# Optimization experiments

Measured on AMD Instinct MI355X. Metric: run time of the kernel, lower is better.

Reference implementation:

```python
import jax, jax.numpy as jnp
import numpy as np

BS, SEQ_LEN, N_NODES = 16, 12, 512
D, H, L, K = 256, 8, 2, 16
DFF = 4 * D
DH = D // H


def setup_inputs() -> dict:
    key = jax.random.key(0)
    ks = jax.random.split(key, 12)
    p = lambda i, shape: jax.random.normal(ks[i], shape, dtype=jnp.float32) * 0.02
    return dict(
        x_c=jax.random.normal(ks[0], (BS, SEQ_LEN, N_NODES), dtype=jnp.float32),
        A=jax.random.uniform(ks[1], (N_NODES, N_NODES), dtype=jnp.float32),
        W_src_emb=p(2, (SEQ_LEN, D)),
        W_tgt_emb=p(3, (SEQ_LEN, D)),
        enc_attn=p(4, (L, 4, D, D)),
        enc_ffn1=p(5, (L, D, DFF)),
        enc_ffn2=p(6, (L, DFF, D)),
        dec_self=p(7, (L, 4, D, D)),
        dec_cross=p(8, (L, 4, D, D)),
        dec_ffn1=p(9, (L, D, DFF)),
        dec_ffn2=p(10, (L, DFF, D)),
        W_gen=p(11, (D, SEQ_LEN)),
    )


def _ln(x):
    m = jnp.mean(x, axis=-1, keepdims=True)
    v = jnp.var(x, axis=-1, keepdims=True)
    return (x - m) * jax.lax.rsqrt(v + 1e-6)


def _mha(xq, xkv, W):
    # xq: [b, n, q, D], xkv: [b, n, s, D], W: [4, D, D]
    q = (xq @ W[0]).reshape(xq.shape[:-1] + (H, DH))
    k = (xkv @ W[1]).reshape(xkv.shape[:-1] + (H, DH))
    v = (xkv @ W[2]).reshape(xkv.shape[:-1] + (H, DH))
    sc = jnp.einsum('bnqhe,bnkhe->bnhqk', q, k) / np.float32(np.sqrt(DH))
    a = jax.nn.softmax(sc, axis=-1)
    o = jnp.einsum('bnhqk,bnkhe->bnqhe', a, v)
    o = o.reshape(o.shape[:-2] + (D,))
    return o @ W[3]


def _pe(length):
    pos = jnp.arange(length, dtype=jnp.float32)[:, None]
    div = jnp.exp(jnp.arange(0, D, 2, dtype=jnp.float32) * (-np.log(10000.0) / D))
    pe = jnp.zeros((length, D), dtype=jnp.float32)
    pe = pe.at[:, 0::2].set(jnp.sin(pos * div)).at[:, 1::2].set(jnp.cos(pos * div))
    return pe


def reference(x_c, A, W_src_emb, W_tgt_emb, enc_attn, enc_ffn1, enc_ffn2,
              dec_self, dec_cross, dec_ffn1, dec_ffn2, W_gen):
    # x_c: [bs, seq_len, N] -> x: [bs, N, seq_len]
    x = jnp.transpose(x_c, (0, 2, 1))
    # top-k neighbors per node (descending by A)
    index = jnp.argsort(-A, axis=-1)[:, :K]            # [N, K]
    sx = x[:, index]                                   # [bs, N, K, seq_len]  (the gather)
    tgt_in = x[:, :, None, :]                          # [bs, N, 1, seq_len]

    scale = np.float32(np.sqrt(D))
    src = sx @ W_src_emb * scale + _pe(K)              # [bs, N, K, D]
    tgt = tgt_in @ W_tgt_emb * scale + _pe(1)          # [bs, N, 1, D]

    # encoder (pre-norm residual sublayers, annotated-transformer style)
    for l in range(L):
        y = _ln(src)
        src = src + _mha(y, y, enc_attn[l])
        y = _ln(src)
        src = src + jax.nn.relu(y @ enc_ffn1[l]) @ enc_ffn2[l]
    memory = _ln(src)

    # decoder
    for l in range(L):
        y = _ln(tgt)
        tgt = tgt + _mha(y, y, dec_self[l])
        y = _ln(tgt)
        tgt = tgt + _mha(y, memory, dec_cross[l])
        y = _ln(tgt)
        tgt = tgt + jax.nn.relu(y @ dec_ffn1[l]) @ dec_ffn2[l]
    out = _ln(tgt) @ W_gen                             # [bs, N, 1, seq_len]
    return out[:, :, 0, :]                             # squeeze(-2): [bs, N, seq_len]
```

## Files before the change

### kernel.cpp

```cpp
#include <hip/hip_runtime.h>

typedef unsigned short u16;
typedef __attribute__((ext_vector_type(8))) short short8;
typedef __attribute__((ext_vector_type(4))) float f32x4;

__device__ __forceinline__ float bf2f(unsigned v){ union{unsigned u; float f;} c; c.u = v<<16; return c.f; }
__device__ __forceinline__ u16 f2bf(float f){
  union{float f; unsigned u;} c; c.f=f;
  unsigned u = c.u;
  u += 0x7fffu + ((u>>16)&1u);
  return (u16)(u>>16);
}

__device__ __forceinline__ float wsum(float v){
  #pragma unroll
  for(int off=32; off>0; off>>=1) v += __shfl_xor(v, off);
  return v;
}

#define GLDS(g, l) __builtin_amdgcn_global_load_lds( \
    (const __attribute__((address_space(1))) void*)(g), \
    (__attribute__((address_space(3))) void*)(l), 16, 0, 0)

__global__ void topk_kernel(const float* __restrict__ A, int* __restrict__ idx){
  __shared__ float vals[512];
  const int n = blockIdx.x, t = threadIdx.x;
  for(int i=t;i<512;i+=64) vals[i] = A[n*512+i];
  __syncthreads();
  for(int kk=0;kk<16;kk++){
    float bv = -1e30f; int bi = 1<<30;
    for(int i=t;i<512;i+=64){
      float v = vals[i];
      if(v > bv){ bv=v; bi=i; }
    }
    #pragma unroll
    for(int off=32; off>0; off>>=1){
      float ov = __shfl_down(bv, off);
      int   oi = __shfl_down(bi, off);
      if(ov > bv || (ov==bv && oi<bi)){ bv=ov; bi=oi; }
    }
    bi = __shfl(bi, 0);
    if(t==0){ idx[n*16+kk] = bi; vals[bi] = -1e30f; }
    __syncthreads();
  }
}

__global__ __launch_bounds__(256)
void tcvt_kernel(const float* __restrict__ src, u16* __restrict__ dst, int R, int C){
  __shared__ float t[32][33];
  const int m = blockIdx.z;
  src += (size_t)m*R*C; dst += (size_t)m*R*C;
  const int c0 = blockIdx.x*32, r0 = blockIdx.y*32;
  const int tx = threadIdx.x, ty = threadIdx.y;
  #pragma unroll
  for(int i=0;i<4;i++) t[ty*4+i][tx] = src[(size_t)(r0+ty*4+i)*C + c0+tx];
  __syncthreads();
  #pragma unroll
  for(int i=0;i<4;i++) dst[(size_t)(c0+ty*4+i)*R + r0+tx] = f2bf(t[tx][ty*4+i]);
}

__global__ void embed_kernel(const float* __restrict__ x_c, const int* __restrict__ idx,
                             const float* __restrict__ Wsrc, const float* __restrict__ Wtgt,
                             u16* __restrict__ S, u16* __restrict__ TGT, int g0){
  __shared__ float xs[16][12];
  __shared__ float xt[12];
  const int gl = blockIdx.x, g = gl + g0, b = g>>9, n = g&511, d = threadIdx.x;
  if(d < 192){ int kk=d/12, t=d-kk*12; xs[kk][t] = x_c[(b*12+t)*512 + idx[n*16+kk]]; }
  else if(d < 204){ int t=d-192; xt[t] = x_c[(b*12+t)*512 + n]; }
  __syncthreads();
  float wsr[12], wtg[12];
  #pragma unroll
  for(int t=0;t<12;t++){ wsr[t]=Wsrc[t*256+d]; wtg[t]=Wtgt[t*256+d]; }
  const float freq = expf(-(float)(d & ~1) * (9.210340371976184f/256.0f));
  const bool odd = d & 1;
  for(int kk=0;kk<16;kk++){
    float a=0;
    #pragma unroll
    for(int t=0;t<12;t++) a = fmaf(xs[kk][t], wsr[t], a);
    float pe = odd ? cosf(freq*(float)kk) : sinf(freq*(float)kk);
    S[(size_t)(gl*16+kk)*256 + d] = f2bf(a*16.0f + pe);
  }
  float a=0;
  #pragma unroll
  for(int t=0;t<12;t++) a = fmaf(xt[t], wtg[t], a);
  TGT[(size_t)gl*256 + d] = f2bf(a*16.0f + (odd?1.0f:0.0f));
}

__global__ __launch_bounds__(256) void ln_kernel(const u16* __restrict__ X, u16* __restrict__ Y){
  const int lane = threadIdx.x & 63, w = threadIdx.x >> 6;
  const size_t row = (size_t)blockIdx.x*4 + w;
  const size_t base = row*256 + (size_t)lane*4;
  ushort4 u = *(const ushort4*)(X + base);
  float x0=bf2f(u.x), x1=bf2f(u.y), x2=bf2f(u.z), x3=bf2f(u.w);
  float mean = wsum(x0+x1+x2+x3) * (1.0f/256.0f);
  float d0=x0-mean, d1=x1-mean, d2=x2-mean, d3=x3-mean;
  float var = wsum(d0*d0+d1*d1+d2*d2+d3*d3) * (1.0f/256.0f);
  float sc = rsqrtf(var + 1e-6f);
  ushort4 o; o.x=f2bf(d0*sc); o.y=f2bf(d1*sc); o.z=f2bf(d2*sc); o.w=f2bf(d3*sc);
  *(ushort4*)(Y + base) = o;
}

template<int MODE>
__global__ __launch_bounds__(256)
void gemm_mfma(const u16* __restrict__ A, const u16* __restrict__ Bt, u16* __restrict__ C,
               int M, int N, int K)
{
  __shared__ u16 As[128*32];
  __shared__ u16 Bs[128*32];
  const int tid = threadIdx.x;
  const int w = tid>>6, l = tid&63;
  const int quad = l>>4, col16 = l&15;
  const int wr = (w>>1)*64, wc = (w&1)*64;
  const size_t m0 = (size_t)blockIdx.x*128;
  const size_t n0 = (size_t)blockIdx.y*128;

  const int sr = l>>2, sc = (l&3)*8;
  const int ca = w*2, cb = w*2+1;
  const u16* aG0 = A  + (m0 + ca*16 + sr)*K + sc;
  const u16* aG1 = A  + (m0 + cb*16 + sr)*K + sc;
  const u16* bG0 = Bt + (n0 + ca*16 + sr)*K + sc;
  const u16* bG1 = Bt + (n0 + cb*16 + sr)*K + sc;
  u16* aL0 = &As[ca*512];
  u16* aL1 = &As[cb*512];
  u16* bL0 = &Bs[ca*512];
  u16* bL1 = &Bs[cb*512];

  f32x4 acc[4][4];
  #pragma unroll
  for(int i=0;i<4;i++)
    #pragma unroll
    for(int j=0;j<4;j++) acc[i][j] = (f32x4){0.f,0.f,0.f,0.f};

  for(int k0=0;k0<K;k0+=32){
    GLDS(aG0 + k0, aL0);
    GLDS(aG1 + k0, aL1);
    GLDS(bG0 + k0, bL0);
    GLDS(bG1 + k0, bL1);
    __syncthreads();
    short8 af[4], bf[4];
    #pragma unroll
    for(int i=0;i<4;i++) af[i] = *(const short8*)&As[(wr + i*16 + col16)*32 + quad*8];
    #pragma unroll
    for(int j=0;j<4;j++) bf[j] = *(const short8*)&Bs[(wc + j*16 + col16)*32 + quad*8];
    #pragma unroll
    for(int i=0;i<4;i++)
      #pragma unroll
      for(int j=0;j<4;j++)
        acc[i][j] = __builtin_amdgcn_mfma_f32_16x16x32_bf16(af[i], bf[j], acc[i][j], 0,0,0);
    __syncthreads();
  }

  #pragma unroll
  for(int i=0;i<4;i++){
    #pragma unroll
    for(int r=0;r<4;r++){
      const size_t row = m0 + wr + i*16 + quad*4 + r;
      u16* cp = C + row*(size_t)N + n0 + wc + col16;
      #pragma unroll
      for(int j=0;j<4;j++){
        float v = acc[i][j][r];
        if(MODE==2) v += bf2f(cp[j*16]);
        if(MODE==1) v = fmaxf(v, 0.f);
        cp[j*16] = f2bf(v);
      }
    }
  }
}

__global__ __launch_bounds__(128)
void attn_enc_kernel(const u16* __restrict__ QKV, u16* __restrict__ O){
  __shared__ float qs[16*264], ks[16*264], vs[16*264];
  const size_t grow = (size_t)blockIdx.x*16;
  for(int i=threadIdx.x;i<4096;i+=128){
    int r=i>>8, c=i&255;
    int li = r*264 + ((c>>5)*33) + (c&31);
    const u16* p = QKV + (grow+r)*768 + c;
    qs[li]=bf2f(p[0]); ks[li]=bf2f(p[256]); vs[li]=bf2f(p[512]);
  }
  __syncthreads();
  const int h = threadIdx.x>>4, q = threadIdx.x&15;
  const int ho = h*33;
  float sc[16];
  for(int kk=0;kk<16;kk++){
    float s=0;
    const float* qp = &qs[q*264+ho];
    const float* kp = &ks[kk*264+ho];
    #pragma unroll
    for(int e=0;e<32;e++) s = fmaf(qp[e], kp[e], s);
    sc[kk] = s*0.17677669529663687f;
  }
  float m=sc[0];
  #pragma unroll
  for(int kk=1;kk<16;kk++) m=fmaxf(m,sc[kk]);
  float sum=0;
  #pragma unroll
  for(int kk=0;kk<16;kk++){ sc[kk]=expf(sc[kk]-m); sum+=sc[kk]; }
  float inv=1.0f/sum;
  for(int e=0;e<32;e++){
    float o=0;
    #pragma unroll
    for(int kk=0;kk<16;kk++) o = fmaf(sc[kk], vs[kk*264+ho+e], o);
    O[(grow+q)*256 + h*32 + e] = f2bf(o*inv);
  }
}

__global__ __launch_bounds__(256)
void attn_cross_kernel(const u16* __restrict__ Qc, const u16* __restrict__ KV,
                       u16* __restrict__ Oc){
  __shared__ float qs[256];
  __shared__ float ks[16*264], vs[16*264];
  __shared__ float aw[128];
  const int t = threadIdx.x;
  const size_t g = blockIdx.x;
  qs[t] = bf2f(Qc[g*256+t]);
  for(int i=t;i<4096;i+=256){
    int r=i>>8, c=i&255;
    int li = r*264 + ((c>>5)*33) + (c&31);
    const u16* p = KV + (g*16+r)*512 + c;
    ks[li]=bf2f(p[0]); vs[li]=bf2f(p[256]);
  }
  __syncthreads();
  if(t<128){
    int h=t>>4, kk=t&15;
    float s=0;
    #pragma unroll
    for(int e=0;e<32;e++) s = fmaf(qs[h*32+e], ks[kk*264+h*33+e], s);
    aw[h*16+kk] = s*0.17677669529663687f;
  }
  __syncthreads();
  if(t<8){
    float m=-1e30f;
    for(int kk=0;kk<16;kk++) m=fmaxf(m, aw[t*16+kk]);
    float sum=0;
    for(int kk=0;kk<16;kk++){ float e=expf(aw[t*16+kk]-m); aw[t*16+kk]=e; sum+=e; }
    float inv=1.0f/sum;
    for(int kk=0;kk<16;kk++) aw[t*16+kk]*=inv;
  }
  __syncthreads();
  {
    int h=t>>5, e=t&31;
    float o=0;
    #pragma unroll
    for(int kk=0;kk<16;kk++) o = fmaf(aw[h*16+kk], vs[kk*264+h*33+e], o);
    Oc[g*256+t] = f2bf(o);
  }
}

__global__ __launch_bounds__(64)
void final_kernel(const u16* __restrict__ T, const float* __restrict__ Wg, float* __restrict__ out, int g0){
  __shared__ float y[256];
  const int lane = threadIdx.x;
  const size_t gl = blockIdx.x;
  ushort4 u = *(const ushort4*)(T + gl*256 + (size_t)lane*4);
  float x0=bf2f(u.x), x1=bf2f(u.y), x2=bf2f(u.z), x3=bf2f(u.w);
  float mean = wsum(x0+x1+x2+x3)*(1.0f/256.0f);
  float d0=x0-mean,d1=x1-mean,d2=x2-mean,d3=x3-mean;
  float var = wsum(d0*d0+d1*d1+d2*d2+d3*d3)*(1.0f/256.0f);
  float sc = rsqrtf(var+1e-6f);
  y[lane*4+0]=d0*sc; y[lane*4+1]=d1*sc; y[lane*4+2]=d2*sc; y[lane*4+3]=d3*sc;
  __syncthreads();
  if(lane<12){
    float s=0;
    for(int d=0;d<256;d++) s = fmaf(y[d], Wg[d*12+lane], s);
    out[(g0+gl)*12+lane]=s;
  }
}

extern "C" void kernel_launch(void* const* d_in, const int* in_sizes, int n_in,
                              void* d_out, int out_size, void* d_ws, size_t ws_size,
                              hipStream_t stream)
{
  (void)in_sizes; (void)n_in; (void)out_size;
  const float* x_c  = (const float*)d_in[0];
  const float* A    = (const float*)d_in[1];
  const float* Wsrc = (const float*)d_in[2];
  const float* Wtgt = (const float*)d_in[3];
  const float* wsrc_f[7] = {(const float*)d_in[4],(const float*)d_in[5],(const float*)d_in[6],
                            (const float*)d_in[7],(const float*)d_in[8],(const float*)d_in[9],
                            (const float*)d_in[10]};
  const float* W_gen = (const float*)d_in[11];
  float* out = (float*)d_out;

  auto align256 = [](size_t b)->size_t{ return (b + 255) & ~(size_t)255; };
  auto need_bytes = [&](int GC)->size_t{
    size_t b = 0;
    b += align256(512*16*4);
    for(int i=0;i<7;i++) b += align256((size_t)524288*2);
    b += align256((size_t)GC*16*256*2)*2;
    b += align256((size_t)GC*16*1024*2);
    b += align256((size_t)GC*256*2)*4;
    b += align256((size_t)GC*1024*2);
    return b;
  };
  int GC = 8192;
  while(GC > 128 && need_bytes(GC) > ws_size) GC >>= 1;

  char* ws = (char*)d_ws;
  size_t off = 0;
  auto alloc = [&](size_t bytes)->char*{
    char* p = ws + off;
    off += (bytes + 255) & ~(size_t)255;
    return p;
  };
  int* idx = (int*)alloc(512*16*4);
  u16* wt[7];
  for(int i=0;i<7;i++) wt[i] = (u16*)alloc((size_t)524288*2);
  u16* cS  = (u16*)alloc((size_t)GC*16*256*2);
  u16* cY  = (u16*)alloc((size_t)GC*16*256*2);
  u16* big = (u16*)alloc((size_t)GC*16*1024*2);
  u16* tgt = (u16*)alloc((size_t)GC*256*2);
  u16* tY  = (u16*)alloc((size_t)GC*256*2);
  u16* tA  = (u16*)alloc((size_t)GC*256*2);
  u16* tO  = (u16*)alloc((size_t)GC*256*2);
  u16* tT  = (u16*)alloc((size_t)GC*1024*2);

  u16* wQKV = big;
  u16* Tc   = big;
  u16* KVc  = big;

  {
    dim3 blk(32,8);
    tcvt_kernel<<<dim3( 256/32, 256/32, 8), blk, 0, stream>>>(wsrc_f[0], wt[0], 256, 256);
    tcvt_kernel<<<dim3(1024/32, 256/32, 2), blk, 0, stream>>>(wsrc_f[1], wt[1], 256,1024);
    tcvt_kernel<<<dim3( 256/32,1024/32, 2), blk, 0, stream>>>(wsrc_f[2], wt[2],1024, 256);
    tcvt_kernel<<<dim3( 256/32, 256/32, 8), blk, 0, stream>>>(wsrc_f[3], wt[3], 256, 256);
    tcvt_kernel<<<dim3( 256/32, 256/32, 8), blk, 0, stream>>>(wsrc_f[4], wt[4], 256, 256);
    tcvt_kernel<<<dim3(1024/32, 256/32, 2), blk, 0, stream>>>(wsrc_f[5], wt[5], 256,1024);
    tcvt_kernel<<<dim3( 256/32,1024/32, 2), blk, 0, stream>>>(wsrc_f[6], wt[6],1024, 256);
  }
  topk_kernel<<<512,64,0,stream>>>(A, idx);

  auto gemm = [&](const u16* Am, const u16* Bm, u16* Cm, int M_, int N_, int K_, int mode){
    dim3 grid(M_/128, N_/128);
    if(mode==1)      gemm_mfma<1><<<grid,256,0,stream>>>(Am,Bm,Cm,M_,N_,K_);
    else if(mode==2) gemm_mfma<2><<<grid,256,0,stream>>>(Am,Bm,Cm,M_,N_,K_);
    else             gemm_mfma<0><<<grid,256,0,stream>>>(Am,Bm,Cm,M_,N_,K_);
  };

  const int Mr = GC*16;
  const int Md = GC;

  for(int g0=0; g0<8192; g0+=GC){
    embed_kernel<<<GC,256,0,stream>>>(x_c, idx, Wsrc, Wtgt, cS, tgt, g0);

    for(int l=0;l<2;l++){
      const u16* Wat = wt[0] + (size_t)l*4*65536;
      ln_kernel<<<Mr/4,256,0,stream>>>(cS, cY);
      gemm(cY, Wat,           wQKV, Mr, 768, 256, 0);
      attn_enc_kernel<<<GC,128,0,stream>>>(wQKV, cY);
      gemm(cY, Wat+3*65536,   cS,   Mr, 256, 256, 2);
      ln_kernel<<<Mr/4,256,0,stream>>>(cS, cY);
      gemm(cY, wt[1]+(size_t)l*262144, Tc, Mr,1024, 256, 1);
      gemm(Tc, wt[2]+(size_t)l*262144, cS, Mr, 256,1024, 2);
    }
    ln_kernel<<<Mr/4,256,0,stream>>>(cS, cY);

    for(int l=0;l<2;l++){
      const u16* Wds = wt[3] + (size_t)l*4*65536;
      const u16* Wdc = wt[4] + (size_t)l*4*65536;
      ln_kernel<<<Md/4,256,0,stream>>>(tgt, tY);
      gemm(tY, Wds+2*65536, tA,  Md, 256, 256, 0);
      gemm(tA, Wds+3*65536, tgt, Md, 256, 256, 2);
      ln_kernel<<<Md/4,256,0,stream>>>(tgt, tY);
      gemm(tY, Wdc,          tA,  Md, 256, 256, 0);
      gemm(cY, Wdc+1*65536,  KVc, Mr, 512, 256, 0);
      attn_cross_kernel<<<GC,256,0,stream>>>(tA, KVc, tO);
      gemm(tO, Wdc+3*65536,  tgt, Md, 256, 256, 2);
      ln_kernel<<<Md/4,256,0,stream>>>(tgt, tY);
      gemm(tY, wt[5]+(size_t)l*262144, tT,  Md,1024, 256, 1);
      gemm(tT, wt[6]+(size_t)l*262144, tgt, Md, 256,1024, 2);
    }

    final_kernel<<<GC,64,0,stream>>>(tgt, W_gen, out, g0);
  }
}
```

Measured before the change: 2.032 ms.

## Fold decoder self-attn V·O weights, batch cross KV GEMM, vectorize LN and attention

With a single target token, decoder self-attention reduces to V then O, so the two 256x256 weights are premultiplied into one matrix, removing one GEMM per decoder layer. The cross-attention K/V projections for both layers are packed into one weight and computed in a single N=1024 GEMM, with the attention kernel indexing by layer offset. LayerNorm now processes 8 rows per block with 16-byte loads. Encoder attention keeps bf16 in LDS, holds q and output in registers and runs two groups per block. Premultiplying the weights adds an extra bf16 rounding step that may shift accuracy slightly.

```diff
diff --git a/kernel.cpp b/kernel.cpp
--- a/kernel.cpp
+++ b/kernel.cpp
@@ -1,6 +1,7 @@
 #include <hip/hip_runtime.h>
 
 typedef unsigned short u16;
+typedef unsigned int u32;
 typedef __attribute__((ext_vector_type(8))) short short8;
 typedef __attribute__((ext_vector_type(4))) float f32x4;
 
@@ -11,10 +12,13 @@
   u += 0x7fffu + ((u>>16)&1u);
   return (u16)(u>>16);
 }
-
-__device__ __forceinline__ float wsum(float v){
-  #pragma unroll
-  for(int off=32; off>0; off>>=1) v += __shfl_xor(v, off);
+__device__ __forceinline__ float bfLO(u32 x){ union{u32 u; float f;} c; c.u = x<<16;        return c.f; }
+__device__ __forceinline__ float bfHI(u32 x){ union{u32 u; float f;} c; c.u = x&0xffff0000u; return c.f; }
+__device__ __forceinline__ u32 pack2(float a, float b){ return (u32)f2bf(a) | ((u32)f2bf(b)<<16); }
+
+__device__ __forceinline__ float hsum32(float v){
+  #pragma unroll
+  for(int off=16; off>0; off>>=1) v += __shfl_xor(v, off);
   return v;
 }
 
@@ -57,6 +61,14 @@
   __syncthreads();
   #pragma unroll
   for(int i=0;i<4;i++) dst[(size_t)(c0+ty*4+i)*R + r0+tx] = f2bf(t[tx][ty*4+i]);
+}
+
+__global__ void cvt_kernel(const float* __restrict__ in, u16* __restrict__ out, int n4){
+  int i = blockIdx.x*256 + threadIdx.x;
+  if(i>=n4) return;
+  float4 v = ((const float4*)in)[i];
+  ushort4 o; o.x=f2bf(v.x); o.y=f2bf(v.y); o.z=f2bf(v.z); o.w=f2bf(v.w);
+  ((ushort4*)out)[i] = o;
 }
 
 __global__ void embed_kernel(const float* __restrict__ x_c, const int* __restrict__ idx,
@@ -87,17 +99,26 @@
 }
 
 __global__ __launch_bounds__(256) void ln_kernel(const u16* __restrict__ X, u16* __restrict__ Y){
-  const int lane = threadIdx.x & 63, w = threadIdx.x >> 6;
-  const size_t row = (size_t)blockIdx.x*4 + w;
-  const size_t base = row*256 + (size_t)lane*4;
-  ushort4 u = *(const ushort4*)(X + base);
-  float x0=bf2f(u.x), x1=bf2f(u.y), x2=bf2f(u.z), x3=bf2f(u.w);
-  float mean = wsum(x0+x1+x2+x3) * (1.0f/256.0f);
-  float d0=x0-mean, d1=x1-mean, d2=x2-mean, d3=x3-mean;
-  float var = wsum(d0*d0+d1*d1+d2*d2+d3*d3) * (1.0f/256.0f);
-  float sc = rsqrtf(var + 1e-6f);
-  ushort4 o; o.x=f2bf(d0*sc); o.y=f2bf(d1*sc); o.z=f2bf(d2*sc); o.w=f2bf(d3*sc);
-  *(ushort4*)(Y + base) = o;
+  const int tid = threadIdx.x;
+  const int lh = tid & 31;
+  const size_t row = (size_t)blockIdx.x*8 + (tid>>5);
+  const size_t base = row*256 + (size_t)lh*8;
+  uint4 u = *(const uint4*)(X + base);
+  float x[8];
+  x[0]=bfLO(u.x); x[1]=bfHI(u.x); x[2]=bfLO(u.y); x[3]=bfHI(u.y);
+  x[4]=bfLO(u.z); x[5]=bfHI(u.z); x[6]=bfLO(u.w); x[7]=bfHI(u.w);
+  float s=0;
+  #pragma unroll
+  for(int i=0;i<8;i++) s += x[i];
+  float mean = hsum32(s) * (1.0f/256.0f);
+  float v=0;
+  #pragma unroll
+  for(int i=0;i<8;i++){ x[i]-=mean; v += x[i]*x[i]; }
+  float sc = rsqrtf(hsum32(v)*(1.0f/256.0f) + 1e-6f);
+  uint4 o;
+  o.x = pack2(x[0]*sc, x[1]*sc); o.y = pack2(x[2]*sc, x[3]*sc);
+  o.z = pack2(x[4]*sc, x[5]*sc); o.w = pack2(x[6]*sc, x[7]*sc);
+  *(uint4*)(Y + base) = o;
 }
 
 template<int MODE>
@@ -167,26 +188,41 @@
   }
 }
 
-__global__ __launch_bounds__(128)
+__global__ __launch_bounds__(256)
 void attn_enc_kernel(const u16* __restrict__ QKV, u16* __restrict__ O){
-  __shared__ float qs[16*264], ks[16*264], vs[16*264];
-  const size_t grow = (size_t)blockIdx.x*16;
-  for(int i=threadIdx.x;i<4096;i+=128){
-    int r=i>>8, c=i&255;
-    int li = r*264 + ((c>>5)*33) + (c&31);
-    const u16* p = QKV + (grow+r)*768 + c;
-    qs[li]=bf2f(p[0]); ks[li]=bf2f(p[256]); vs[li]=bf2f(p[512]);
-  }
-  __syncthreads();
-  const int h = threadIdx.x>>4, q = threadIdx.x&15;
-  const int ho = h*33;
+  __shared__ u16 sh[2][12672];
+  const int tid = threadIdx.x;
+  const int half = tid>>7, th = tid&127;
+  const size_t g = (size_t)blockIdx.x*2 + half;
+  const size_t grow = g*16;
+  u16* sb = sh[half];
+  #pragma unroll
+  for(int it=0; it<12; it++){
+    int e = (th + 128*it)*8;
+    int r = e/768, c = e - r*768;
+    int t = c>>8, cc = c&255;
+    *(uint4*)&sb[t*4224 + r*264 + cc] = *(const uint4*)&QKV[(grow+r)*768 + c];
+  }
+  __syncthreads();
+  const int h = th>>4, q = th&15;
+  const int ho = h*32;
+  float qv[32];
+  #pragma unroll
+  for(int e2=0;e2<16;e2++){
+    u32 x = *(const u32*)&sb[q*264 + ho + e2*2];
+    qv[2*e2]=bfLO(x); qv[2*e2+1]=bfHI(x);
+  }
   float sc[16];
+  #pragma unroll
   for(int kk=0;kk<16;kk++){
+    const u16* kr = &sb[4224 + kk*264 + ho];
     float s=0;
-    const float* qp = &qs[q*264+ho];
-    const float* kp = &ks[kk*264+ho];
-    #pragma unroll
-    for(int e=0;e<32;e++) s = fmaf(qp[e], kp[e], s);
+    #pragma unroll
+    for(int e2=0;e2<16;e2++){
+      u32 x = *(const u32*)&kr[e2*2];
+      s = fmaf(qv[2*e2], bfLO(x), s);
+      s = fmaf(qv[2*e2+1], bfHI(x), s);
+    }
     sc[kk] = s*0.17677669529663687f;
   }
   float m=sc[0];
@@ -196,17 +232,31 @@
   #pragma unroll
   for(int kk=0;kk<16;kk++){ sc[kk]=expf(sc[kk]-m); sum+=sc[kk]; }
   float inv=1.0f/sum;
-  for(int e=0;e<32;e++){
-    float o=0;
-    #pragma unroll
-    for(int kk=0;kk<16;kk++) o = fmaf(sc[kk], vs[kk*264+ho+e], o);
-    O[(grow+q)*256 + h*32 + e] = f2bf(o*inv);
+  float ov[32];
+  #pragma unroll
+  for(int e=0;e<32;e++) ov[e]=0.f;
+  #pragma unroll
+  for(int kk=0;kk<16;kk++){
+    float p = sc[kk]*inv;
+    const u16* vr = &sb[8448 + kk*264 + ho];
+    #pragma unroll
+    for(int e2=0;e2<16;e2++){
+      u32 x = *(const u32*)&vr[e2*2];
+      ov[2*e2]   = fmaf(p, bfLO(x), ov[2*e2]);
+      ov[2*e2+1] = fmaf(p, bfHI(x), ov[2*e2+1]);
+    }
+  }
+  u16* op = O + (grow+q)*256 + ho;
+  #pragma unroll
+  for(int b=0;b<8;b++){
+    ushort4 t4; t4.x=f2bf(ov[4*b]); t4.y=f2bf(ov[4*b+1]); t4.z=f2bf(ov[4*b+2]); t4.w=f2bf(ov[4*b+3]);
+    *(ushort4*)&op[b*4] = t4;
   }
 }
 
 __global__ __launch_bounds__(256)
 void attn_cross_kernel(const u16* __restrict__ Qc, const u16* __restrict__ KV,
-                       u16* __restrict__ Oc){
+                       u16* __restrict__ Oc, int loff){
   __shared__ float qs[256];
   __shared__ float ks[16*264], vs[16*264];
   __shared__ float aw[128];
@@ -216,7 +266,7 @@
   for(int i=t;i<4096;i+=256){
     int r=i>>8, c=i&255;
     int li = r*264 + ((c>>5)*33) + (c&31);
-    const u16* p = KV + (g*16+r)*512 + c;
+    const u16* p = KV + (g*16+r)*1024 + loff + c;
     ks[li]=bf2f(p[0]); vs[li]=bf2f(p[256]);
   }
   __syncthreads();
@@ -253,10 +303,15 @@
   const size_t gl = blockIdx.x;
   ushort4 u = *(const ushort4*)(T + gl*256 + (size_t)lane*4);
   float x0=bf2f(u.x), x1=bf2f(u.y), x2=bf2f(u.z), x3=bf2f(u.w);
-  float mean = wsum(x0+x1+x2+x3)*(1.0f/256.0f);
+  float s4 = x0+x1+x2+x3;
+  #pragma unroll
+  for(int off=32; off>0; off>>=1) s4 += __shfl_xor(s4, off);
+  float mean = s4*(1.0f/256.0f);
   float d0=x0-mean,d1=x1-mean,d2=x2-mean,d3=x3-mean;
-  float var = wsum(d0*d0+d1*d1+d2*d2+d3*d3)*(1.0f/256.0f);
-  float sc = rsqrtf(var+1e-6f);
+  float v4 = d0*d0+d1*d1+d2*d2+d3*d3;
+  #pragma unroll
+  for(int off=32; off>0; off>>=1) v4 += __shfl_xor(v4, off);
+  float sc = rsqrtf(v4*(1.0f/256.0f)+1e-6f);
   y[lane*4+0]=d0*sc; y[lane*4+1]=d1*sc; y[lane*4+2]=d2*sc; y[lane*4+3]=d3*sc;
   __syncthreads();
   if(lane<12){
@@ -286,6 +341,8 @@
     size_t b = 0;
     b += align256(512*16*4);
     for(int i=0;i<7;i++) b += align256((size_t)524288*2);
+    b += align256((size_t)4*65536*2);
+    b += align256((size_t)2*65536*2)*2;
     b += align256((size_t)GC*16*256*2)*2;
     b += align256((size_t)GC*16*1024*2);
     b += align256((size_t)GC*256*2)*4;
@@ -305,6 +362,9 @@
   int* idx = (int*)alloc(512*16*4);
   u16* wt[7];
   for(int i=0;i<7;i++) wt[i] = (u16*)alloc((size_t)524288*2);
+  u16* wKV      = (u16*)alloc((size_t)4*65536*2);
+  u16* wv_plain = (u16*)alloc((size_t)2*65536*2);
+  u16* wVO      = (u16*)alloc((size_t)2*65536*2);
   u16* cS  = (u16*)alloc((size_t)GC*16*256*2);
   u16* cY  = (u16*)alloc((size_t)GC*16*256*2);
   u16* big = (u16*)alloc((size_t)GC*16*1024*2);
@@ -330,6 +390,17 @@
   }
   topk_kernel<<<512,64,0,stream>>>(A, idx);
 
+  hipMemcpyAsync(wKV+0*65536, wt[4]+1*65536, 65536*2, hipMemcpyDeviceToDevice, stream);
+  hipMemcpyAsync(wKV+1*65536, wt[4]+2*65536, 65536*2, hipMemcpyDeviceToDevice, stream);
+  hipMemcpyAsync(wKV+2*65536, wt[4]+5*65536, 65536*2, hipMemcpyDeviceToDevice, stream);
+  hipMemcpyAsync(wKV+3*65536, wt[4]+6*65536, 65536*2, hipMemcpyDeviceToDevice, stream);
+
+  for(int l=0;l<2;l++){
+    cvt_kernel<<<64,256,0,stream>>>(wsrc_f[3]+(size_t)(l*4+2)*65536, wv_plain+(size_t)l*65536, 16384);
+    gemm_mfma<0><<<dim3(2,2),256,0,stream>>>(wt[3]+(size_t)(l*4+3)*65536, wv_plain+(size_t)l*65536,
+                                             wVO+(size_t)l*65536, 256,256,256);
+  }
+
   auto gemm = [&](const u16* Am, const u16* Bm, u16* Cm, int M_, int N_, int K_, int mode){
     dim3 grid(M_/128, N_/128);
     if(mode==1)      gemm_mfma<1><<<grid,256,0,stream>>>(Am,Bm,Cm,M_,N_,K_);
@@ -345,28 +416,26 @@
 
     for(int l=0;l<2;l++){
       const u16* Wat = wt[0] + (size_t)l*4*65536;
-      ln_kernel<<<Mr/4,256,0,stream>>>(cS, cY);
+      ln_kernel<<<Mr/8,256,0,stream>>>(cS, cY);
       gemm(cY, Wat,           wQKV, Mr, 768, 256, 0);
-      attn_enc_kernel<<<GC,128,0,stream>>>(wQKV, cY);
+      attn_enc_kernel<<<GC/2,256,0,stream>>>(wQKV, cY);
       gemm(cY, Wat+3*65536,   cS,   Mr, 256, 256, 2);
-      ln_kernel<<<Mr/4,256,0,stream>>>(cS, cY);
+      ln_kernel<<<Mr/8,256,0,stream>>>(cS, cY);
       gemm(cY, wt[1]+(size_t)l*262144, Tc, Mr,1024, 256, 1);
       gemm(Tc, wt[2]+(size_t)l*262144, cS, Mr, 256,1024, 2);
     }
-    ln_kernel<<<Mr/4,256,0,stream>>>(cS, cY);
+    ln_kernel<<<Mr/8,256,0,stream>>>(cS, cY);
+    gemm(cY, wKV, KVc, Mr, 1024, 256, 0);
 
     for(int l=0;l<2;l++){
-      const u16* Wds = wt[3] + (size_t)l*4*65536;
       const u16* Wdc = wt[4] + (size_t)l*4*65536;
-      ln_kernel<<<Md/4,256,0,stream>>>(tgt, tY);
-      gemm(tY, Wds+2*65536, tA,  Md, 256, 256, 0);
-      gemm(tA, Wds+3*65536, tgt, Md, 256, 256, 2);
-      ln_kernel<<<Md/4,256,0,stream>>>(tgt, tY);
+      ln_kernel<<<Md/8,256,0,stream>>>(tgt, tY);
+      gemm(tY, wVO+(size_t)l*65536, tgt, Md, 256, 256, 2);
+      ln_kernel<<<Md/8,256,0,stream>>>(tgt, tY);
       gemm(tY, Wdc,          tA,  Md, 256, 256, 0);
-      gemm(cY, Wdc+1*65536,  KVc, Mr, 512, 256, 0);
-      attn_cross_kernel<<<GC,256,0,stream>>>(tA, KVc, tO);
+      attn_cross_kernel<<<GC,256,0,stream>>>(tA, KVc, tO, l*512);
       gemm(tO, Wdc+3*65536,  tgt, Md, 256, 256, 2);
-      ln_kernel<<<Md/4,256,0,stream>>>(tgt, tY);
+      ln_kernel<<<Md/8,256,0,stream>>>(tgt, tY);
       gemm(tY, wt[5]+(size_t)l*262144, tT,  Md,1024, 256, 1);
       gemm(tT, wt[6]+(size_t)l*262144, tgt, Md, 256,1024, 2);
     }
```

Result: faster. 1.902 ms (-6.4%).
